# Optimization experiments

Hardware: AMD Instinct MI355X
Metric: run time of the kernel (lower is better)

## Reference

```python
import jax, jax.numpy as jnp
import numpy as np

N = 2
GRIDS = [(512, 512), (256, 256), (128, 128), (64, 64), (32, 32)]
STRIDES = [4, 8, 16, 32, 64]
SIZES = [32, 64, 128, 256, 512]
ASPECTS = (0.5, 1.0, 2.0)
A = len(ASPECTS)
IMG_H = IMG_W = 2048
PRE_NMS = 1000      # pre_nms_top_n['testing']
POST_NMS = 1000     # post_nms_top_n['testing']
NMS_THRESH = 0.7
SCORE_THRESH = 0.0
MIN_SIZE = 1e-3
BBOX_XFORM_CLIP = float(np.log(1000.0 / 16.0))  # torchvision BoxCoder clamp


def _make_anchors():
    """AnchorGenerator.grid_anchors for each level; returns list of [H*W*A, 4]."""
    ar = jnp.asarray(ASPECTS, jnp.float32)
    hr = jnp.sqrt(ar)
    wr = 1.0 / hr
    levels = []
    for (gh, gw), s, size in zip(GRIDS, STRIDES, SIZES):
        ws = wr * size
        hs = hr * size
        base = jnp.round(jnp.stack([-ws, -hs, ws, hs], 1) / 2.0)  # [A,4]
        sx = (jnp.arange(gw) * s).astype(jnp.float32)
        sy = (jnp.arange(gh) * s).astype(jnp.float32)
        yy, xx = jnp.meshgrid(sy, sx, indexing='ij')
        shifts = jnp.stack([xx.ravel(), yy.ravel(), xx.ravel(), yy.ravel()], 1)
        levels.append((shifts[:, None, :] + base[None, :, :]).reshape(-1, 4))
    return levels


def _flatten_obj(o):
    # permute_and_flatten with C=1: [N,A,H,W] -> [N, H*W*A]
    n, ac, h, w = o.shape
    return o.reshape(n, ac, 1, h, w).transpose(0, 3, 4, 1, 2).reshape(n, -1)


def _flatten_box(b):
    # permute_and_flatten with C=4: [N,A*4,H,W] -> [N, H*W*A, 4]
    n, a4, h, w = b.shape
    return b.reshape(n, a4 // 4, 4, h, w).transpose(0, 3, 4, 1, 2).reshape(n, -1, 4)


def _decode(deltas, anchors):
    # BoxCoder.decode with weights (1,1,1,1); deltas [N,M,4], anchors [M,4]
    wa = anchors[:, 2] - anchors[:, 0]
    ha = anchors[:, 3] - anchors[:, 1]
    cxa = anchors[:, 0] + 0.5 * wa
    cya = anchors[:, 1] + 0.5 * ha
    dx, dy = deltas[..., 0], deltas[..., 1]
    dw = jnp.minimum(deltas[..., 2], BBOX_XFORM_CLIP)
    dh = jnp.minimum(deltas[..., 3], BBOX_XFORM_CLIP)
    cx = dx * wa + cxa
    cy = dy * ha + cya
    w = jnp.exp(dw) * wa
    h = jnp.exp(dh) * ha
    return jnp.stack([cx - 0.5 * w, cy - 0.5 * h, cx + 0.5 * w, cy + 0.5 * h], -1)


def _nms_select(boxes, scores, n_out, thresh):
    """Greedy NMS returning fixed n_out (index, valid) pairs. boxes [K,4]."""
    area = jnp.maximum(boxes[:, 2] - boxes[:, 0], 0.0) * jnp.maximum(boxes[:, 3] - boxes[:, 1], 0.0)

    def step(s, _):
        i = jnp.argmax(s)
        valid = s[i] > -jnp.inf
        b = boxes[i]
        lt = jnp.maximum(boxes[:, :2], b[:2])
        rb = jnp.minimum(boxes[:, 2:], b[2:])
        wh = jnp.maximum(rb - lt, 0.0)
        inter = wh[:, 0] * wh[:, 1]
        iou = inter / (area + area[i] - inter + 1e-9)
        s = jnp.where(iou > thresh, -jnp.inf, s).at[i].set(-jnp.inf)
        return s, (i, valid)

    _, (idx, valid) = jax.lax.scan(step, scores, None, length=n_out)
    return idx, valid


def _rpn_forward(objs, dts):
    anchors = _make_anchors()
    b_all, s_all, l_all = [], [], []
    for li, (o, d, a) in enumerate(zip(objs, dts, anchors)):
        of = _flatten_obj(o)            # [N, HWA]
        df = _flatten_box(d)            # [N, HWA, 4]
        props = _decode(df, a)          # [N, HWA, 4]
        k = min(PRE_NMS, of.shape[1])
        ts, ti = jax.lax.top_k(of, k)   # top-k on raw objectness (per level)
        b_all.append(jnp.take_along_axis(props, ti[..., None], 1))
        s_all.append(ts)
        l_all.append(jnp.full((of.shape[0], k), float(li), jnp.float32))
    boxes = jnp.concatenate(b_all, 1)   # [N, K, 4]
    raw = jnp.concatenate(s_all, 1)     # [N, K]
    lvl = jnp.concatenate(l_all, 1)     # [N, K]

    def per_image(bx, rs, lv):
        sc = jax.nn.sigmoid(rs)
        x1 = jnp.clip(bx[:, 0], 0.0, IMG_W)
        y1 = jnp.clip(bx[:, 1], 0.0, IMG_H)
        x2 = jnp.clip(bx[:, 2], 0.0, IMG_W)
        y2 = jnp.clip(bx[:, 3], 0.0, IMG_H)
        bx = jnp.stack([x1, y1, x2, y2], 1)
        keep = ((x2 - x1) >= MIN_SIZE) & ((y2 - y1) >= MIN_SIZE) & (sc > SCORE_THRESH)
        ms = jnp.where(keep, sc, -jnp.inf)
        off = lv * (IMG_W + IMG_H + 1.0)  # batched_nms level offset
        idx, valid = _nms_select(jax.lax.stop_gradient(bx + off[:, None]),
                                 jax.lax.stop_gradient(ms), POST_NMS, NMS_THRESH)
        v = valid.astype(bx.dtype)
        ob = bx[idx] * v[:, None]
        os = sc[idx] * v
        return jnp.concatenate([ob, os[:, None]], 1)  # [POST_NMS, 5]

    return jax.vmap(per_image)(boxes, raw, lvl)       # [N, POST_NMS, 5]


def setup_inputs() -> dict:
    key = jax.random.key(0)
    ks = jax.random.split(key, 10)
    inp = {}
    for i, (gh, gw) in enumerate(GRIDS):
        inp[f"obj{i}"] = jax.random.normal(ks[i], (N, A, gh, gw), jnp.float32)
        inp[f"box{i}"] = jax.random.normal(ks[5 + i], (N, A * 4, gh, gw), jnp.float32) * 0.5
    return inp


def reference(obj0, obj1, obj2, obj3, obj4, box0, box1, box2, box3, box4):
    return _rpn_forward([obj0, obj1, obj2, obj3, obj4],
                        [box0, box1, box2, box3, box4])
```

## Files before the change

kernel.cpp:

```cpp
#include <hip/hip_runtime.h>
#include <cmath>

#pragma clang fp contract(off)

typedef unsigned int u32;
typedef unsigned short u16;
typedef unsigned long long u64;

#define K_PER_LVL 1000
#define KTOT 5000
#define NIMG 2
#define BINS 16384
#define BIN_SHIFT 18
#define SEGW (BINS / 256)
#define EQ_CAP 2048
#define ECAP 32768
#define LECAP 24576
#define CBUF 1024
#define RNK_IB 512
#define RNK_JB 250
#define RNK_NJ (KTOT / RNK_JB)
#define RNK_TILES 200
#define EDGE_TILES 820

__constant__ int c_LG[5] = {512, 256, 128, 64, 32};
__constant__ int c_LS[5] = {4, 8, 16, 32, 64};
__constant__ int c_LZ[5] = {32, 64, 128, 256, 512};
__constant__ int c_LM[5] = {786432, 196608, 49152, 12288, 3072};

struct Ptrs { const float* o[5]; const float* b[5]; };

__device__ inline u32 fkey(float f) {
    u32 u = __float_as_uint(f);
    return (u & 0x80000000u) ? ~u : (u | 0x80000000u);
}

__global__ __launch_bounds__(256) void k_zero(u32* __restrict__ z, int nwords) {
    int i = blockIdx.x * 256 + threadIdx.x;
    int stride = gridDim.x * 256;
    for (; i < nwords; i += stride) z[i] = 0;
}

__global__ __launch_bounds__(256) void k_hist(Ptrs P, u32* __restrict__ hist) {
    int p = blockIdx.y; int l = p % 5; int n = p / 5;
    int M4 = c_LM[l] >> 2;
    const float4* base = (const float4*)(P.o[l] + (size_t)n * c_LM[l]);
    __shared__ u32 lh[BINS];
    for (int i = threadIdx.x; i < BINS; i += 256) lh[i] = 0;
    __syncthreads();
    int stride = gridDim.x * 256;
    for (int i = blockIdx.x * 256 + threadIdx.x; i < M4; i += stride) {
        float4 v = base[i];
        atomicAdd(&lh[fkey(v.x) >> BIN_SHIFT], 1u);
        atomicAdd(&lh[fkey(v.y) >> BIN_SHIFT], 1u);
        atomicAdd(&lh[fkey(v.z) >> BIN_SHIFT], 1u);
        atomicAdd(&lh[fkey(v.w) >> BIN_SHIFT], 1u);
    }
    __syncthreads();
    for (int i = threadIdx.x; i < BINS; i += 256) {
        u32 c = lh[i];
        if (c) atomicAdd(&hist[p * BINS + i], c);
    }
}

__global__ __launch_bounds__(256) void k_resolve(const u32* __restrict__ hist,
                                                 int* __restrict__ binB, int* __restrict__ kneed,
                                                 int* __restrict__ g0) {
    int p = blockIdx.x, t = threadIdx.x;
    __shared__ u32 seg[256];
    __shared__ u32 tail[SEGW];
    __shared__ int sgS; __shared__ u32 GS;
    u32 s = 0;
    const u32* hb = hist + p * BINS;
    int base = t * SEGW;
    for (int q = 0; q < SEGW; ++q) s += hb[base + q];
    seg[t] = s;
    __syncthreads();
    if (t == 0) {
        u32 G = 0; int sg = 255;
        for (; sg > 0; --sg) {
            if (G + seg[sg] >= (u32)K_PER_LVL) break;
            G += seg[sg];
        }
        sgS = sg; GS = G;
    }
    __syncthreads();
    int sg = sgS;
    if (t < SEGW) tail[t] = hb[sg * SEGW + t];
    __syncthreads();
    if (t == 0) {
        u32 G = GS; int B = sg * SEGW;
        for (int b = SEGW - 1; b >= 0; --b) {
            u32 c = tail[b];
            if (G + c >= (u32)K_PER_LVL) { B = sg * SEGW + b; break; }
            G += c;
        }
        binB[p] = B;
        kneed[p] = K_PER_LVL - (int)G;
        g0[p] = (int)G;
    }
}

__global__ __launch_bounds__(256) void k_compact(Ptrs P, const int* __restrict__ binB,
                                                 u32* gcnt, u32* ecnt,
                                                 int* __restrict__ sel, u64* __restrict__ eq) {
    int p = blockIdx.y; int l = p % 5; int n = p / 5;
    int M4 = c_LM[l] >> 2; int gg = c_LM[l] / 3;
    const float4* base = (const float4*)(P.o[l] + (size_t)n * c_LM[l]);
    int B = binB[p];
    __shared__ u32 lsel[CBUF];
    __shared__ u64 leq[CBUF];
    __shared__ u32 cSel, cEq, baseSel, baseEq;
    if (threadIdx.x == 0) { cSel = 0; cEq = 0; }
    __syncthreads();
    int stride = gridDim.x * 256;
    for (int i4 = blockIdx.x * 256 + threadIdx.x; i4 < M4; i4 += stride) {
        float4 v = base[i4];
        float vv[4] = {v.x, v.y, v.z, v.w};
        #pragma unroll
        for (int q = 0; q < 4; ++q) {
            u32 k = fkey(vv[q]);
            int bin = (int)(k >> BIN_SHIFT);
            if (bin < B) continue;
            int i = i4 * 4 + q;
            int a = i / gg; int pix = i - a * gg; int m = pix * 3 + a;
            if (bin > B) {
                u32 t = atomicAdd(&cSel, 1u);
                if (t < CBUF) lsel[t] = (u32)m;
                else { u32 pos = atomicAdd(&gcnt[p], 1u); sel[p * K_PER_LVL + pos] = m; }
            } else {
                u64 pk = ((u64)k << 20) | (u64)(0xFFFFFu ^ (u32)m);
                u32 t = atomicAdd(&cEq, 1u);
                if (t < CBUF) leq[t] = pk;
                else { u32 e = atomicAdd(&ecnt[p], 1u); if (e < EQ_CAP) eq[(size_t)p * EQ_CAP + e] = pk; }
            }
        }
    }
    __syncthreads();
    if (threadIdx.x == 0) {
        u32 ns = cSel < CBUF ? cSel : CBUF;
        u32 ne = cEq < CBUF ? cEq : CBUF;
        baseSel = ns ? atomicAdd(&gcnt[p], ns) : 0u;
        baseEq  = ne ? atomicAdd(&ecnt[p], ne) : 0u;
    }
    __syncthreads();
    u32 ns = cSel < CBUF ? cSel : CBUF;
    u32 ne = cEq < CBUF ? cEq : CBUF;
    for (u32 i = threadIdx.x; i < ns; i += 256) sel[p * K_PER_LVL + baseSel + i] = (int)lsel[i];
    for (u32 i = threadIdx.x; i < ne; i += 256) {
        u32 slot = baseEq + i;
        if (slot < EQ_CAP) eq[(size_t)p * EQ_CAP + slot] = leq[i];
    }
}

__global__ __launch_bounds__(256) void k_eqsel(const u32* __restrict__ ecnt, const int* __restrict__ kneed,
                                               const int* __restrict__ g0,
                                               const u64* __restrict__ eq, int* __restrict__ sel) {
    int p = blockIdx.x, t = threadIdx.x;
    int E = (int)ecnt[p]; if (E > EQ_CAP) E = EQ_CAP;
    int KF = kneed[p]; int G0 = g0[p];
    __shared__ u64 a[EQ_CAP];
    for (int i = t; i < E; i += 256) a[i] = eq[(size_t)p * EQ_CAP + i];
    __syncthreads();
    u64 mine[8]; int rk[8];
    #pragma unroll
    for (int q = 0; q < 8; ++q) {
        int i = t + q * 256;
        mine[q] = (i < E) ? a[i] : 0ULL;
        rk[q] = 0;
    }
    for (int j = 0; j < E; ++j) {
        u64 v = a[j];
        #pragma unroll
        for (int q = 0; q < 8; ++q) rk[q] += (v > mine[q]) ? 1 : 0;
    }
    #pragma unroll
    for (int q = 0; q < 8; ++q) {
        int i = t + q * 256;
        if (i < E && rk[q] < KF) {
            int m = (int)(0xFFFFFu ^ (u32)(mine[q] & 0xFFFFFu));
            sel[p * K_PER_LVL + G0 + rk[q]] = m;
        }
    }
}

__global__ void k_feat(Ptrs P, const int* __restrict__ sel, u64* __restrict__ key64,
                       float* __restrict__ csc, float* __restrict__ cbox, float* __restrict__ cobox) {
    int tid = blockIdx.x * 256 + threadIdx.x;
    if (tid >= NIMG * KTOT) return;
    int p = tid / K_PER_LVL, s = tid - p * K_PER_LVL;
    int n = p / 5, l = p % 5;
    int G = c_LG[l], S = c_LS[l], Z = c_LZ[l];
    int gg = G * G;
    int m = sel[p * K_PER_LVL + s];
    int a = m % 3; int pix = m / 3; int h = pix / G; int w = pix - h * G;

    const float ars[3] = {0.5f, 1.0f, 2.0f};
    float ar = ars[a];
    float hr = sqrtf(ar), wr = 1.0f / hr;
    float wsz = wr * (float)Z, hsz = hr * (float)Z;
    float bx1 = rintf(-0.5f * wsz), by1 = rintf(-0.5f * hsz);
    float bx2 = rintf(0.5f * wsz),  by2 = rintf(0.5f * hsz);
    float sx = (float)(w * S), sy = (float)(h * S);
    float ax1 = sx + bx1, ay1 = sy + by1, ax2 = sx + bx2, ay2 = sy + by2;
    float wa = ax2 - ax1, ha = ay2 - ay1;
    float cxa = ax1 + 0.5f * wa, cya = ay1 + 0.5f * ha;

    const float* bb = P.b[l] + (size_t)n * 12 * gg;
    float dx = bb[(a * 4 + 0) * gg + pix];
    float dy = bb[(a * 4 + 1) * gg + pix];
    const float CLIPV = 4.135166556742356f;
    float dw = fminf(bb[(a * 4 + 2) * gg + pix], CLIPV);
    float dh = fminf(bb[(a * 4 + 3) * gg + pix], CLIPV);
    float cx = dx * wa + cxa, cy = dy * ha + cya;
    float ww = expf(dw) * wa, hh = expf(dh) * ha;
    float x1 = cx - 0.5f * ww, y1 = cy - 0.5f * hh;
    float x2 = cx + 0.5f * ww, y2 = cy + 0.5f * hh;
    x1 = fminf(fmaxf(x1, 0.f), 2048.f);
    y1 = fminf(fmaxf(y1, 0.f), 2048.f);
    x2 = fminf(fmaxf(x2, 0.f), 2048.f);
    y2 = fminf(fmaxf(y2, 0.f), 2048.f);

    float raw = P.o[l][(size_t)n * 3 * gg + a * gg + pix];
    float sc = 1.0f / (1.0f + expf(-raw));
    bool keep = (x2 - x1 >= 1e-3f) && (y2 - y1 >= 1e-3f) && (sc > 0.0f);

    int slot = n * KTOT + l * K_PER_LVL + s;
    u32 tb = ((u32)l << 20) | (u32)m;
    u32 kk = keep ? fkey(raw) : 0u;
    key64[slot] = ((u64)kk << 23) | (u64)(tb ^ 0x7FFFFFu);

    csc[slot] = keep ? sc : -INFINITY;
    cbox[slot * 4 + 0] = x1; cbox[slot * 4 + 1] = y1;
    cbox[slot * 4 + 2] = x2; cbox[slot * 4 + 3] = y2;
    float off = 4097.0f * (float)l;
    cobox[slot * 4 + 0] = x1 + off; cobox[slot * 4 + 1] = y1 + off;
    cobox[slot * 4 + 2] = x2 + off; cobox[slot * 4 + 3] = y2 + off;
}

__global__ __launch_bounds__(256) void k_redge(const u64* __restrict__ key64, u32* __restrict__ rpart,
                                               const float* __restrict__ cobox,
                                               u32* __restrict__ gE, u32* __restrict__ gPairs) {
    int n = blockIdx.y;
    int x = blockIdx.x;
    __shared__ u64 kj[RNK_JB];
    __shared__ float cb[64][4];
    if (x < RNK_TILES) {
        int i0 = (x / 20) * RNK_IB;
        int j0 = (x % 20) * RNK_JB;
        const u64* kb = key64 + (size_t)n * KTOT;
        for (int t = threadIdx.x; t < RNK_JB; t += 256) kj[t] = kb[j0 + t];
        __syncthreads();
        int i1 = i0 + threadIdx.x, i2 = i1 + 256;
        u64 k1 = (i1 < KTOT) ? kb[i1] : ~0ULL;
        u64 k2 = (i2 < KTOT) ? kb[i2] : ~0ULL;
        u32 r1 = 0, r2 = 0;
        #pragma unroll 10
        for (int j = 0; j < RNK_JB; ++j) {
            u64 v = kj[j];
            r1 += (v > k1) ? 1u : 0u;
            r2 += (v > k2) ? 1u : 0u;
        }
        u32* rp = rpart + (size_t)(x % 20) * (NIMG * KTOT) + n * KTOT;
        if (i1 < KTOT) rp[i1] = r1;
        if (i2 < KTOT) rp[i2] = r2;
        return;
    }
    int e = x - RNK_TILES, bi = 0;
    while (true) { int c = 79 - 4 * bi; if (e < c) break; e -= c; ++bi; }
    int bj = 4 * bi + e;
    int i = bi * 256 + threadIdx.x;
    int j0 = bj * 64;
    if (threadIdx.x < 64) {
        int jl = j0 + threadIdx.x;
        if (jl < KTOT) {
            cb[threadIdx.x][0] = cobox[(size_t)(n * KTOT + jl) * 4 + 0];
            cb[threadIdx.x][1] = cobox[(size_t)(n * KTOT + jl) * 4 + 1];
            cb[threadIdx.x][2] = cobox[(size_t)(n * KTOT + jl) * 4 + 2];
            cb[threadIdx.x][3] = cobox[(size_t)(n * KTOT + jl) * 4 + 3];
        } else {
            cb[threadIdx.x][0] = 0.f; cb[threadIdx.x][1] = 0.f;
            cb[threadIdx.x][2] = 0.f; cb[threadIdx.x][3] = 0.f;
        }
    }
    __syncthreads();
    if (i >= KTOT) return;
    float x1 = cobox[(size_t)(n * KTOT + i) * 4 + 0];
    float y1 = cobox[(size_t)(n * KTOT + i) * 4 + 1];
    float x2 = cobox[(size_t)(n * KTOT + i) * 4 + 2];
    float y2 = cobox[(size_t)(n * KTOT + i) * 4 + 3];
    float areai = fmaxf(x2 - x1, 0.f) * fmaxf(y2 - y1, 0.f);
    int lim = KTOT - j0; if (lim > 64) lim = 64;
    for (int jj = 0; jj < lim; ++jj) {
        int j = j0 + jj;
        if (j <= i) continue;
        float bx1 = cb[jj][0], by1 = cb[jj][1], bx2 = cb[jj][2], by2 = cb[jj][3];
        float areaj = fmaxf(bx2 - bx1, 0.f) * fmaxf(by2 - by1, 0.f);
        float ltx = fmaxf(x1, bx1), lty = fmaxf(y1, by1);
        float rbx = fminf(x2, bx2), rby = fminf(y2, by2);
        float iw = fmaxf(rbx - ltx, 0.f), ih = fmaxf(rby - lty, 0.f);
        float inter = iw * ih;
        float iou = inter / (areai + areaj - inter + 1e-9f);
        if (iou > 0.7f) {
            u32 pos = atomicAdd(&gE[n], 1u);
            if (pos < ECAP) gPairs[(size_t)n * ECAP + pos] = ((u32)i << 13) | (u32)j;
        }
    }
}

__global__ __launch_bounds__(256) void k_scat(const u32* __restrict__ rpart, const float* __restrict__ csc,
                       const float* __restrict__ cbox,
                       float* __restrict__ ssc, float* __restrict__ sbox, u32* __restrict__ rankArr) {
    int n = blockIdx.y;
    int i = blockIdx.x * 256 + threadIdx.x;
    if (i >= KTOT) return;
    int idx = n * KTOT + i;
    u32 rank = 0;
    #pragma unroll
    for (int jb = 0; jb < RNK_NJ; ++jb) rank += rpart[(size_t)jb * (NIMG * KTOT) + idx];
    rankArr[idx] = rank;
    int src = idx, dst = n * KTOT + (int)rank;
    ssc[dst] = csc[src];
    sbox[dst * 4 + 0] = cbox[src * 4 + 0]; sbox[dst * 4 + 1] = cbox[src * 4 + 1];
    sbox[dst * 4 + 2] = cbox[src * 4 + 2]; sbox[dst * 4 + 3] = cbox[src * 4 + 3];
}

__global__ __launch_bounds__(256, 1) void k_nms(const float* __restrict__ ssc,
                      const float* __restrict__ sbox, const u32* __restrict__ rankArr,
                      const u32* __restrict__ gE, const u32* __restrict__ gPairs,
                      u16* __restrict__ gEdges, float* __restrict__ out) {
    int n = blockIdx.x, tid = threadIdx.x;
    int lane = tid & 63, wv = tid >> 6;
    __shared__ u32 cnt[KTOT];
    __shared__ u32 offs[KTOT + 1];
    __shared__ u16 edges[LECAP];
    __shared__ u32 rem32[160];
    __shared__ u32 colLo[64], colHi[64];
    __shared__ u32 scanb[256];
    __shared__ int picksS;

    for (int i = tid; i < KTOT; i += 256) cnt[i] = 0;
    if (tid < 160) rem32[tid] = 0xFFFFFFFFu;
    __syncthreads();
    for (int w = wv; w < 79; w += 4) {
        int i = w * 64 + lane;
        bool dead = (i >= KTOT) || !(ssc[n * KTOT + i] > -INFINITY);
        u64 db = __ballot(dead);
        if (lane == 0) { rem32[2 * w] = (u32)db; rem32[2 * w + 1] = (u32)(db >> 32); }
    }
    __syncthreads();

    int E = (int)gE[n]; if (E > ECAP) E = ECAP;
    for (int k = tid; k < E; k += 256) {
        u32 p = gPairs[(size_t)n * ECAP + k];
        u32 ra = rankArr[n * KTOT + (p >> 13)], rb = rankArr[n * KTOT + (p & 0x1FFFu)];
        u32 src = ra < rb ? ra : rb;
        atomicAdd(&cnt[src], 1u);
    }
    __syncthreads();
    u32 s = 0; int base = tid * 20;
    if (tid < 250) for (int q = 0; q < 20; ++q) s += cnt[base + q];
    scanb[tid] = s;
    __syncthreads();
    for (int off = 1; off < 256; off <<= 1) {
        u32 v = (tid >= off) ? scanb[tid - off] : 0;
        __syncthreads();
        scanb[tid] += v;
        __syncthreads();
    }
    u32 tbase = (tid == 0) ? 0u : scanb[tid - 1];
    if (tid < 250) {
        u32 run = tbase;
        for (int q = 0; q < 20; ++q) { offs[base + q] = run; run += cnt[base + q]; }
    }
    if (tid == 0) offs[KTOT] = scanb[255];
    __syncthreads();
    for (int i = tid; i < KTOT; i += 256) cnt[i] = 0;
    __syncthreads();
    for (int k = tid; k < E; k += 256) {
        u32 p = gPairs[(size_t)n * ECAP + k];
        u32 ra = rankArr[n * KTOT + (p >> 13)], rb = rankArr[n * KTOT + (p & 0x1FFFu)];
        u32 src = ra < rb ? ra : rb, dst = ra < rb ? rb : ra;
        u32 slot = offs[src] + atomicAdd(&cnt[src], 1u);
        if (slot < LECAP) edges[slot] = (u16)dst;
        else gEdges[(size_t)n * ECAP + slot] = (u16)dst;
    }
    __syncthreads();

    if (wv == 0) {
        int picks = 0;
        for (int w = 0; w < 79 && picks < 1000; ++w) {
            u64 rw = ((u64)rem32[2 * w + 1] << 32) | rem32[2 * w];
            u64 alive = ~rw;
            if (alive == 0ULL) continue;
            int c = w * 64 + lane;
            bool amAlive = ((alive >> lane) & 1ULL) != 0ULL;
            int e0 = 0, e1 = 0;
            if (amAlive) { e0 = (int)offs[c]; e1 = (int)offs[c + 1]; }
            colLo[lane] = 0; colHi[lane] = 0;
            bool anyIntra = false;
            for (int k = e0; k < e1; ++k) {
                int dst = (k < LECAP) ? (int)edges[k] : (int)gEdges[(size_t)n * ECAP + k];
                if ((dst >> 6) == w) {
                    if (lane < 32) atomicOr(&colLo[dst & 63], 1u << lane);
                    else           atomicOr(&colHi[dst & 63], 1u << (lane - 32));
                    anyIntra = true;
                }
            }
            u64 cm;
            if (__ballot(anyIntra) == 0ULL) {
                cm = alive;
            } else {
                u64 col = ((u64)colHi[lane] << 32) | colLo[lane];
                cm = 0ULL;
                for (int e = 0; e < 64; ++e) {
                    if (!((alive >> e) & 1ULL)) continue;
                    u64 ce = __shfl(col, e);
                    if ((cm & ce) == 0ULL) cm |= (1ULL << e);
                }
            }
            int allowed = 1000 - picks;
            int ncom = __popcll(cm);
            while (ncom > allowed) { cm &= ~(1ULL << (63 - __clzll(cm))); --ncom; }
            if ((cm >> lane) & 1ULL) {
                int pos = picks + (int)__popcll(cm & ((1ULL << lane) - 1ULL));
                const float* bp = &sbox[(size_t)(n * KTOT + c) * 4];
                float* op = &out[(n * 1000 + pos) * 5];
                op[0] = bp[0]; op[1] = bp[1]; op[2] = bp[2]; op[3] = bp[3];
                op[4] = ssc[n * KTOT + c];
                for (int k = e0; k < e1; ++k) {
                    int dst = (k < LECAP) ? (int)edges[k] : (int)gEdges[(size_t)n * ECAP + k];
                    atomicOr(&rem32[dst >> 5], 1u << (dst & 31));
                }
            }
            picks += ncom;
        }
        if (lane == 0) picksS = picks;
    }
    __syncthreads();
    int picksF = picksS;
    int basec = (n * 1000 + picksF) * 5, cntz = (1000 - picksF) * 5;
    for (int t = tid; t < cntz; t += 256) out[basec + t] = 0.f;
}

constexpr size_t OFF_HIST   = 0;
constexpr size_t OFF_GCNT   = OFF_HIST + 10 * BINS * 4;
constexpr size_t OFF_ECNT   = OFF_GCNT + 64;
constexpr size_t OFF_GEC    = OFF_ECNT + 64;
constexpr size_t ZERO_WORDS = (10 * BINS * 4 + 192) / 4;
constexpr size_t OFF_BINB   = OFF_GEC + 64;
constexpr size_t OFF_KNEED  = OFF_BINB + 64;
constexpr size_t OFF_G0     = OFF_KNEED + 64;
constexpr size_t OFF_SEL    = OFF_G0 + 64;
constexpr size_t OFF_EQ     = OFF_SEL + 10 * K_PER_LVL * 4;
constexpr size_t OFF_KEY64  = OFF_EQ + (size_t)10 * EQ_CAP * 8;
constexpr size_t OFF_CSC    = OFF_KEY64 + (size_t)NIMG * KTOT * 8;
constexpr size_t OFF_CBOX   = OFF_CSC + (size_t)NIMG * KTOT * 4;
constexpr size_t OFF_COBOX  = OFF_CBOX + (size_t)NIMG * KTOT * 16;
constexpr size_t OFF_SSC    = OFF_COBOX + (size_t)NIMG * KTOT * 16;
constexpr size_t OFF_SBOX   = OFF_SSC + (size_t)NIMG * KTOT * 4;
constexpr size_t OFF_RANK   = OFF_SBOX + (size_t)NIMG * KTOT * 16;
constexpr size_t OFF_PAIRS  = OFF_RANK + (size_t)NIMG * KTOT * 4;
constexpr size_t OFF_ESPILL = OFF_PAIRS + (size_t)NIMG * ECAP * 4;
constexpr size_t OFF_RPART  = OFF_ESPILL + (size_t)NIMG * ECAP * 2;
constexpr size_t WS_NEEDED  = OFF_RPART + (size_t)RNK_NJ * NIMG * KTOT * 4;

extern "C" void kernel_launch(void* const* d_in, const int* in_sizes, int n_in,
                              void* d_out, int out_size, void* d_ws, size_t ws_size,
                              hipStream_t stream) {
    if (ws_size < WS_NEEDED) return;

    bool dictOrder = (in_sizes[1] > in_sizes[0]);
    Ptrs P;
    for (int l = 0; l < 5; ++l) {
        P.o[l] = (const float*)d_in[dictOrder ? (2 * l)     : l];
        P.b[l] = (const float*)d_in[dictOrder ? (2 * l + 1) : (5 + l)];
    }
    char* ws = (char*)d_ws;
    u32*   hist   = (u32*)(ws + OFF_HIST);
    u32*   gcnt   = (u32*)(ws + OFF_GCNT);
    u32*   ecnt   = (u32*)(ws + OFF_ECNT);
    u32*   gec    = (u32*)(ws + OFF_GEC);
    int*   binB   = (int*)(ws + OFF_BINB);
    int*   kneed  = (int*)(ws + OFF_KNEED);
    int*   g0     = (int*)(ws + OFF_G0);
    int*   sel    = (int*)(ws + OFF_SEL);
    u64*   eq     = (u64*)(ws + OFF_EQ);
    u64*   key64  = (u64*)(ws + OFF_KEY64);
    float* csc    = (float*)(ws + OFF_CSC);
    float* cbox   = (float*)(ws + OFF_CBOX);
    float* cobox  = (float*)(ws + OFF_COBOX);
    float* ssc    = (float*)(ws + OFF_SSC);
    float* sbox   = (float*)(ws + OFF_SBOX);
    u32*   rankA  = (u32*)(ws + OFF_RANK);
    u32*   pairs  = (u32*)(ws + OFF_PAIRS);
    u16*   espill = (u16*)(ws + OFF_ESPILL);
    u32*   rpart  = (u32*)(ws + OFF_RPART);
    float* out    = (float*)d_out;

    k_zero<<<dim3(64), 256, 0, stream>>>(hist, (int)ZERO_WORDS);
    k_hist<<<dim3(32, 10), 256, 0, stream>>>(P, hist);
    k_resolve<<<10, 256, 0, stream>>>(hist, binB, kneed, g0);
    k_compact<<<dim3(64, 10), 256, 0, stream>>>(P, binB, gcnt, ecnt, sel, eq);
    k_eqsel<<<10, 256, 0, stream>>>(ecnt, kneed, g0, eq, sel);
    k_feat<<<dim3((NIMG * KTOT + 255) / 256), 256, 0, stream>>>(P, sel, key64, csc, cbox, cobox);
    k_redge<<<dim3(RNK_TILES + EDGE_TILES, NIMG), 256, 0, stream>>>(key64, rpart, cobox, gec, pairs);
    k_scat<<<dim3((KTOT + 255) / 256, NIMG), 256, 0, stream>>>(rpart, csc, cbox, ssc, sbox, rankA);
    k_nms<<<NIMG, 256, 0, stream>>>(ssc, sbox, rankA, gec, pairs, espill, out);
}
```

Baseline: 199.3 us.

## Fuse tie-break selection with feature decode and cache ranked edge pairs in NMS

Merges the equal-key tie-break kernel and the feature/decode kernel into one launch. Ten blocks resolve tied candidates and decode them directly, while forty blocks decode the already-selected candidates, which removes a launch and the round-trip through sel for tied entries. In NMS, the first edge pass writes the rank-remapped (src,dst) pair back into gPairs so the second pass skips the rankArr gathers. The intra-word greedy loop now iterates only over set alive bits using ctz. The trade-off is a serialized tie-break tail inside the fused kernel and an extra global write per edge.

```diff
diff --git a/kernel.cpp b/kernel.cpp
--- a/kernel.cpp
+++ b/kernel.cpp
@@ -33,6 +33,57 @@
 __device__ inline u32 fkey(float f) {
     u32 u = __float_as_uint(f);
     return (u & 0x80000000u) ? ~u : (u | 0x80000000u);
+}
+
+__device__ inline void featOne(const Ptrs& P, int p, int s, int m,
+                               u64* __restrict__ key64, float* __restrict__ csc,
+                               float* __restrict__ cbox, float* __restrict__ cobox) {
+    int n = p / 5, l = p % 5;
+    int G = c_LG[l], S = c_LS[l], Z = c_LZ[l];
+    int gg = G * G;
+    int a = m % 3; int pix = m / 3; int h = pix / G; int w = pix - h * G;
+
+    const float ars[3] = {0.5f, 1.0f, 2.0f};
+    float ar = ars[a];
+    float hr = sqrtf(ar), wr = 1.0f / hr;
+    float wsz = wr * (float)Z, hsz = hr * (float)Z;
+    float bx1 = rintf(-0.5f * wsz), by1 = rintf(-0.5f * hsz);
+    float bx2 = rintf(0.5f * wsz),  by2 = rintf(0.5f * hsz);
+    float sx = (float)(w * S), sy = (float)(h * S);
+    float ax1 = sx + bx1, ay1 = sy + by1, ax2 = sx + bx2, ay2 = sy + by2;
+    float wa = ax2 - ax1, ha = ay2 - ay1;
+    float cxa = ax1 + 0.5f * wa, cya = ay1 + 0.5f * ha;
+
+    const float* bb = P.b[l] + (size_t)n * 12 * gg;
+    float dx = bb[(a * 4 + 0) * gg + pix];
+    float dy = bb[(a * 4 + 1) * gg + pix];
+    const float CLIPV = 4.135166556742356f;
+    float dw = fminf(bb[(a * 4 + 2) * gg + pix], CLIPV);
+    float dh = fminf(bb[(a * 4 + 3) * gg + pix], CLIPV);
+    float cx = dx * wa + cxa, cy = dy * ha + cya;
+    float ww = expf(dw) * wa, hh = expf(dh) * ha;
+    float x1 = cx - 0.5f * ww, y1 = cy - 0.5f * hh;
+    float x2 = cx + 0.5f * ww, y2 = cy + 0.5f * hh;
+    x1 = fminf(fmaxf(x1, 0.f), 2048.f);
+    y1 = fminf(fmaxf(y1, 0.f), 2048.f);
+    x2 = fminf(fmaxf(x2, 0.f), 2048.f);
+    y2 = fminf(fmaxf(y2, 0.f), 2048.f);
+
+    float raw = P.o[l][(size_t)n * 3 * gg + a * gg + pix];
+    float sc = 1.0f / (1.0f + expf(-raw));
+    bool keep = (x2 - x1 >= 1e-3f) && (y2 - y1 >= 1e-3f) && (sc > 0.0f);
+
+    int slot = n * KTOT + l * K_PER_LVL + s;
+    u32 tb = ((u32)l << 20) | (u32)m;
+    u32 kk = keep ? fkey(raw) : 0u;
+    key64[slot] = ((u64)kk << 23) | (u64)(tb ^ 0x7FFFFFu);
+
+    csc[slot] = keep ? sc : -INFINITY;
+    cbox[slot * 4 + 0] = x1; cbox[slot * 4 + 1] = y1;
+    cbox[slot * 4 + 2] = x2; cbox[slot * 4 + 3] = y2;
+    float off = 4097.0f * (float)l;
+    cobox[slot * 4 + 0] = x1 + off; cobox[slot * 4 + 1] = y1 + off;
+    cobox[slot * 4 + 2] = x2 + off; cobox[slot * 4 + 3] = y2 + off;
 }
 
 __global__ __launch_bounds__(256) void k_zero(u32* __restrict__ z, int nwords) {
@@ -153,89 +204,45 @@
     }
 }
 
-__global__ __launch_bounds__(256) void k_eqsel(const u32* __restrict__ ecnt, const int* __restrict__ kneed,
-                                               const int* __restrict__ g0,
-                                               const u64* __restrict__ eq, int* __restrict__ sel) {
-    int p = blockIdx.x, t = threadIdx.x;
-    int E = (int)ecnt[p]; if (E > EQ_CAP) E = EQ_CAP;
-    int KF = kneed[p]; int G0 = g0[p];
-    __shared__ u64 a[EQ_CAP];
-    for (int i = t; i < E; i += 256) a[i] = eq[(size_t)p * EQ_CAP + i];
-    __syncthreads();
-    u64 mine[8]; int rk[8];
-    #pragma unroll
-    for (int q = 0; q < 8; ++q) {
-        int i = t + q * 256;
-        mine[q] = (i < E) ? a[i] : 0ULL;
-        rk[q] = 0;
-    }
-    for (int j = 0; j < E; ++j) {
-        u64 v = a[j];
+__global__ __launch_bounds__(256) void k_eqfeat(Ptrs P, const u32* __restrict__ ecnt,
+                       const int* __restrict__ kneed, const int* __restrict__ g0,
+                       const u64* __restrict__ eq, const int* __restrict__ sel,
+                       u64* __restrict__ key64, float* __restrict__ csc,
+                       float* __restrict__ cbox, float* __restrict__ cobox) {
+    int b = blockIdx.x, t = threadIdx.x;
+    if (b < 10) {
+        int p = b;
+        int E = (int)ecnt[p]; if (E > EQ_CAP) E = EQ_CAP;
+        int KF = kneed[p]; int G0 = g0[p];
+        __shared__ u64 a[EQ_CAP];
+        for (int i = t; i < E; i += 256) a[i] = eq[(size_t)p * EQ_CAP + i];
+        __syncthreads();
+        u64 mine[8]; int rk[8];
         #pragma unroll
-        for (int q = 0; q < 8; ++q) rk[q] += (v > mine[q]) ? 1 : 0;
-    }
-    #pragma unroll
-    for (int q = 0; q < 8; ++q) {
-        int i = t + q * 256;
-        if (i < E && rk[q] < KF) {
-            int m = (int)(0xFFFFFu ^ (u32)(mine[q] & 0xFFFFFu));
-            sel[p * K_PER_LVL + G0 + rk[q]] = m;
-        }
-    }
-}
-
-__global__ void k_feat(Ptrs P, const int* __restrict__ sel, u64* __restrict__ key64,
-                       float* __restrict__ csc, float* __restrict__ cbox, float* __restrict__ cobox) {
-    int tid = blockIdx.x * 256 + threadIdx.x;
-    if (tid >= NIMG * KTOT) return;
-    int p = tid / K_PER_LVL, s = tid - p * K_PER_LVL;
-    int n = p / 5, l = p % 5;
-    int G = c_LG[l], S = c_LS[l], Z = c_LZ[l];
-    int gg = G * G;
-    int m = sel[p * K_PER_LVL + s];
-    int a = m % 3; int pix = m / 3; int h = pix / G; int w = pix - h * G;
-
-    const float ars[3] = {0.5f, 1.0f, 2.0f};
-    float ar = ars[a];
-    float hr = sqrtf(ar), wr = 1.0f / hr;
-    float wsz = wr * (float)Z, hsz = hr * (float)Z;
-    float bx1 = rintf(-0.5f * wsz), by1 = rintf(-0.5f * hsz);
-    float bx2 = rintf(0.5f * wsz),  by2 = rintf(0.5f * hsz);
-    float sx = (float)(w * S), sy = (float)(h * S);
-    float ax1 = sx + bx1, ay1 = sy + by1, ax2 = sx + bx2, ay2 = sy + by2;
-    float wa = ax2 - ax1, ha = ay2 - ay1;
-    float cxa = ax1 + 0.5f * wa, cya = ay1 + 0.5f * ha;
-
-    const float* bb = P.b[l] + (size_t)n * 12 * gg;
-    float dx = bb[(a * 4 + 0) * gg + pix];
-    float dy = bb[(a * 4 + 1) * gg + pix];
-    const float CLIPV = 4.135166556742356f;
-    float dw = fminf(bb[(a * 4 + 2) * gg + pix], CLIPV);
-    float dh = fminf(bb[(a * 4 + 3) * gg + pix], CLIPV);
-    float cx = dx * wa + cxa, cy = dy * ha + cya;
-    float ww = expf(dw) * wa, hh = expf(dh) * ha;
-    float x1 = cx - 0.5f * ww, y1 = cy - 0.5f * hh;
-    float x2 = cx + 0.5f * ww, y2 = cy + 0.5f * hh;
-    x1 = fminf(fmaxf(x1, 0.f), 2048.f);
-    y1 = fminf(fmaxf(y1, 0.f), 2048.f);
-    x2 = fminf(fmaxf(x2, 0.f), 2048.f);
-    y2 = fminf(fmaxf(y2, 0.f), 2048.f);
-
-    float raw = P.o[l][(size_t)n * 3 * gg + a * gg + pix];
-    float sc = 1.0f / (1.0f + expf(-raw));
-    bool keep = (x2 - x1 >= 1e-3f) && (y2 - y1 >= 1e-3f) && (sc > 0.0f);
-
-    int slot = n * KTOT + l * K_PER_LVL + s;
-    u32 tb = ((u32)l << 20) | (u32)m;
-    u32 kk = keep ? fkey(raw) : 0u;
-    key64[slot] = ((u64)kk << 23) | (u64)(tb ^ 0x7FFFFFu);
-
-    csc[slot] = keep ? sc : -INFINITY;
-    cbox[slot * 4 + 0] = x1; cbox[slot * 4 + 1] = y1;
-    cbox[slot * 4 + 2] = x2; cbox[slot * 4 + 3] = y2;
-    float off = 4097.0f * (float)l;
-    cobox[slot * 4 + 0] = x1 + off; cobox[slot * 4 + 1] = y1 + off;
-    cobox[slot * 4 + 2] = x2 + off; cobox[slot * 4 + 3] = y2 + off;
+        for (int q = 0; q < 8; ++q) {
+            int i = t + q * 256;
+            mine[q] = (i < E) ? a[i] : 0ULL;
+            rk[q] = 0;
+        }
+        for (int j = 0; j < E; ++j) {
+            u64 v = a[j];
+            #pragma unroll
+            for (int q = 0; q < 8; ++q) rk[q] += (v > mine[q]) ? 1 : 0;
+        }
+        #pragma unroll
+        for (int q = 0; q < 8; ++q) {
+            int i = t + q * 256;
+            if (i < E && rk[q] < KF) {
+                int m = (int)(0xFFFFFu ^ (u32)(mine[q] & 0xFFFFFu));
+                featOne(P, p, G0 + rk[q], m, key64, csc, cbox, cobox);
+            }
+        }
+    } else {
+        for (int idx = (b - 10) * 256 + t; idx < 10 * K_PER_LVL; idx += 40 * 256) {
+            int p = idx / K_PER_LVL, s = idx - p * K_PER_LVL;
+            if (s < g0[p]) featOne(P, p, s, sel[p * K_PER_LVL + s], key64, csc, cbox, cobox);
+        }
+    }
 }
 
 __global__ __launch_bounds__(256) void k_redge(const u64* __restrict__ key64, u32* __restrict__ rpart,
@@ -327,7 +334,7 @@
 
 __global__ __launch_bounds__(256, 1) void k_nms(const float* __restrict__ ssc,
                       const float* __restrict__ sbox, const u32* __restrict__ rankArr,
-                      const u32* __restrict__ gE, const u32* __restrict__ gPairs,
+                      const u32* __restrict__ gE, u32* __restrict__ gPairs,
                       u16* __restrict__ gEdges, float* __restrict__ out) {
     int n = blockIdx.x, tid = threadIdx.x;
     int lane = tid & 63, wv = tid >> 6;
@@ -354,7 +361,8 @@
     for (int k = tid; k < E; k += 256) {
         u32 p = gPairs[(size_t)n * ECAP + k];
         u32 ra = rankArr[n * KTOT + (p >> 13)], rb = rankArr[n * KTOT + (p & 0x1FFFu)];
-        u32 src = ra < rb ? ra : rb;
+        u32 src = ra < rb ? ra : rb, dst = ra < rb ? rb : ra;
+        gPairs[(size_t)n * ECAP + k] = (src << 13) | dst;
         atomicAdd(&cnt[src], 1u);
     }
     __syncthreads();
@@ -379,8 +387,7 @@
     __syncthreads();
     for (int k = tid; k < E; k += 256) {
         u32 p = gPairs[(size_t)n * ECAP + k];
-        u32 ra = rankArr[n * KTOT + (p >> 13)], rb = rankArr[n * KTOT + (p & 0x1FFFu)];
-        u32 src = ra < rb ? ra : rb, dst = ra < rb ? rb : ra;
+        u32 src = p >> 13, dst = p & 0x1FFFu;
         u32 slot = offs[src] + atomicAdd(&cnt[src], 1u);
         if (slot < LECAP) edges[slot] = (u16)dst;
         else gEdges[(size_t)n * ECAP + slot] = (u16)dst;
@@ -413,8 +420,10 @@
             } else {
                 u64 col = ((u64)colHi[lane] << 32) | colLo[lane];
                 cm = 0ULL;
-                for (int e = 0; e < 64; ++e) {
-                    if (!((alive >> e) & 1ULL)) continue;
+                u64 remb = alive;
+                while (remb) {
+                    int e = __builtin_ctzll(remb);
+                    remb &= remb - 1ULL;
                     u64 ce = __shfl(col, e);
                     if ((cm & ce) == 0ULL) cm |= (1ULL << e);
                 }
@@ -502,8 +511,7 @@
     k_hist<<<dim3(32, 10), 256, 0, stream>>>(P, hist);
     k_resolve<<<10, 256, 0, stream>>>(hist, binB, kneed, g0);
     k_compact<<<dim3(64, 10), 256, 0, stream>>>(P, binB, gcnt, ecnt, sel, eq);
-    k_eqsel<<<10, 256, 0, stream>>>(ecnt, kneed, g0, eq, sel);
-    k_feat<<<dim3((NIMG * KTOT + 255) / 256), 256, 0, stream>>>(P, sel, key64, csc, cbox, cobox);
+    k_eqfeat<<<50, 256, 0, stream>>>(P, ecnt, kneed, g0, eq, sel, key64, csc, cbox, cobox);
     k_redge<<<dim3(RNK_TILES + EDGE_TILES, NIMG), 256, 0, stream>>>(key64, rpart, cobox, gec, pairs);
     k_scat<<<dim3((KTOT + 255) / 256, NIMG), 256, 0, stream>>>(rpart, csc, cbox, ssc, sbox, rankA);
     k_nms<<<NIMG, 256, 0, stream>>>(ssc, sbox, rankA, gec, pairs, espill, out);
```

After: 195.9 us. Within noise of the previous version (-1.7%).
